# Optimization experiments

Measured on AMD Instinct MI355X. Metric: run time of the kernel, lower is better.

The kernel has to match this reference:

```python
import jax, jax.numpy as jnp
import numpy as np

N_NODES = 100000
N_EDGES = 1600000
D_IN = 128
D_H = 128
D_OUT = 64


def _glorot(key, shape):
    fan_in, fan_out = shape[0], shape[1]
    lim = np.sqrt(6.0 / (fan_in + fan_out)).astype(np.float32)
    return jax.random.uniform(key, shape, jnp.float32, -lim, lim)


def setup_inputs() -> dict:
    key = jax.random.key(0)
    ks = jax.random.split(key, 12)
    x = jax.random.normal(ks[0], (N_NODES, D_IN), jnp.float32)
    edge_index = jax.random.randint(ks[1], (2, N_EDGES), 0, N_NODES, jnp.int64)
    return {
        'x': x,
        'edge_index': edge_index,
        'Wl0': _glorot(ks[2], (D_IN, D_H)),  'bl0': jnp.zeros((D_H,), jnp.float32), 'Wr0': _glorot(ks[3], (D_IN, D_H)),
        'Wl1': _glorot(ks[4], (D_H, D_H)),   'bl1': jnp.zeros((D_H,), jnp.float32), 'Wr1': _glorot(ks[5], (D_H, D_H)),
        'Wl2': _glorot(ks[6], (D_H, D_H)),   'bl2': jnp.zeros((D_H,), jnp.float32), 'Wr2': _glorot(ks[7], (D_H, D_H)),
        'W':   _glorot(ks[8], (D_H, D_OUT)), 'b':   jnp.zeros((D_OUT,), jnp.float32),
    }


def _sage_conv(x, src, dst, inv_deg, Wl, bl, Wr):
    # mean aggregation of neighbor features at dst, then lin_l(agg) + lin_r(x)
    agg = jax.ops.segment_sum(x[src], dst, num_segments=N_NODES)  # [N, d]
    mean = agg * inv_deg  # [N, d]
    return mean @ Wl + bl + x @ Wr


def reference(x, edge_index, Wl0, bl0, Wr0, Wl1, bl1, Wr1, Wl2, bl2, Wr2, W, b):
    src, dst = edge_index[0], edge_index[1]
    deg = jax.ops.segment_sum(jnp.ones((N_EDGES,), jnp.float32), dst, num_segments=N_NODES)
    inv_deg = (1.0 / jnp.maximum(deg, 1.0))[:, None]  # [N, 1]
    h = jax.nn.relu(_sage_conv(x, src, dst, inv_deg, Wl0, bl0, Wr0))
    h = jax.nn.relu(_sage_conv(h, src, dst, inv_deg, Wl1, bl1, Wr1))
    h = jax.nn.relu(_sage_conv(h, src, dst, inv_deg, Wl2, bl2, Wr2))
    return h @ W + b
```

## Files before the change

kernel.cpp:

```cpp
#include <hip/hip_runtime.h>
#include <cstddef>

#define N_NODES 100000
#define N_EDGES 1600000
#define D 128
#define NB 782
#define CAP 3072
#define NBLK 1000
#define CHUNK 1600
#define OROW 784
#define WTOT (6 * 16384 + 8192)

typedef unsigned int u32;
typedef unsigned long long u64;
typedef float f32x4 __attribute__((ext_vector_type(4)));
typedef _Float16 f16x8 __attribute__((ext_vector_type(8)));

__device__ inline f16x8 mk16(u64 a, u64 b) {
  union { u64 q[2]; f16x8 v; } u;
  u.q[0] = a; u.q[1] = b;
  return u.v;
}

__device__ inline void acc8(float* a, uint2 d, float c) {
  a[0] += (float)(d.x & 0xFFu) * c;
  a[1] += (float)((d.x >> 8) & 0xFFu) * c;
  a[2] += (float)((d.x >> 16) & 0xFFu) * c;
  a[3] += (float)(d.x >> 24) * c;
  a[4] += (float)(d.y & 0xFFu) * c;
  a[5] += (float)((d.y >> 8) & 0xFFu) * c;
  a[6] += (float)((d.y >> 16) & 0xFFu) * c;
  a[7] += (float)(d.y >> 24) * c;
}


__global__ __launch_bounds__(256) void k_prep(
    const float* __restrict__ x, unsigned short* __restrict__ x16,
    unsigned char* __restrict__ x8, float* __restrict__ sx,
    const float* __restrict__ w0, const float* __restrict__ w1, const float* __restrict__ w2,
    const float* __restrict__ w3, const float* __restrict__ w4, const float* __restrict__ w5,
    const float* __restrict__ w6, unsigned short* __restrict__ wt16) {
  int bid = blockIdx.x;
  int tid = threadIdx.x;
  if (bid < 6250) {
    int row = bid * 16 + (tid >> 4);
    int sub = tid & 15;
    const float* xr = x + (size_t)row * D + sub * 8;
    float4 v0 = *(const float4*)xr;
    float4 v1 = *(const float4*)(xr + 4);
    float vs[8] = {v0.x, v0.y, v0.z, v0.w, v1.x, v1.y, v1.z, v1.w};
    f16x8 h;
#pragma unroll
    for (int j = 0; j < 8; j++) h[j] = (_Float16)vs[j];
    *(uint4*)(x16 + (size_t)row * D + sub * 8) = __builtin_bit_cast(uint4, h);
    float m = 0.f;
#pragma unroll
    for (int j = 0; j < 8; j++) m = fmaxf(m, fabsf(vs[j]));
#pragma unroll
    for (int off = 1; off < 16; off <<= 1) m = fmaxf(m, __shfl_xor(m, off));
    m = fmaxf(m, 1e-8f);
    float inv = 127.0f / m;
    u64 pk = 0;
#pragma unroll
    for (int j = 0; j < 8; j++) {
      int qi = (int)rintf(vs[j] * inv) + 128;
      pk |= (u64)(u32)(qi & 255) << (8 * j);
    }
    *(u64*)(x8 + (size_t)row * D + sub * 8) = pk;
    if (sub == 0) sx[row] = m / 127.0f;
    return;
  }
  int i = (bid - 6250) * 256 + tid;
  if (i >= WTOT) return;
  float v;
  if (i < 6 * 16384) {
    int m = i >> 14;
    int j = i & 16383;
    int c = j >> 7, k = j & 127;
    const float* w = (m == 0) ? w0 : (m == 1) ? w1 : (m == 2) ? w2
                   : (m == 3) ? w3 : (m == 4) ? w4 : w5;
    v = w[k * 128 + c];
  } else {
    int j = i - 6 * 16384;
    int c = j >> 7, k = j & 127;
    v = w6[k * 64 + c];
  }
  _Float16 h = (_Float16)v;
  wt16[i] = __builtin_bit_cast(unsigned short, h);
}


__global__ __launch_bounds__(256) void k_scatter(const int* __restrict__ src,
                                                 const int* __restrict__ dst,
                                                 u32* __restrict__ binned,
                                                 u32* __restrict__ offs) {
  __shared__ int cnt[NB];
  __shared__ int lbase[NB + 1];
  __shared__ int wsum[256];
  __shared__ u32 stage[CHUNK];
  const int tid = threadIdx.x;
  for (int i = tid; i < NB; i += 256) cnt[i] = 0;
  __syncthreads();
  const int e0 = blockIdx.x * CHUNK;
  for (int e = e0 + tid; e < e0 + CHUNK; e += 256)
    atomicAdd(&cnt[dst[e] >> 7], 1);
  __syncthreads();
  int c[4], s = 0;
#pragma unroll
  for (int j = 0; j < 4; j++) {
    int i = tid * 4 + j;
    c[j] = (i < NB) ? cnt[i] : 0;
    s += c[j];
  }
  wsum[tid] = s;
  __syncthreads();
  for (int off = 1; off < 256; off <<= 1) {
    int t = (tid >= off) ? wsum[tid - off] : 0;
    __syncthreads();
    wsum[tid] += t;
    __syncthreads();
  }
  int run = wsum[tid] - s;
#pragma unroll
  for (int j = 0; j < 4; j++) {
    int i = tid * 4 + j;
    if (i < NB) { lbase[i] = run; run += c[j]; }
  }
  if (tid == 0) lbase[NB] = CHUNK;
  __syncthreads();
  for (int i = tid; i < NB; i += 256) cnt[i] = 0;
  __syncthreads();
  for (int e = e0 + tid; e < e0 + CHUNK; e += 256) {
    int d = dst[e];
    int bkt = d >> 7;
    int l = atomicAdd(&cnt[bkt], 1);
    stage[lbase[bkt] + l] = ((u32)(d & 127) << 17) | (u32)src[e];
  }
  u32* orow = offs + (size_t)blockIdx.x * OROW;
  for (int i = tid; i <= NB; i += 256) orow[i] = (u32)lbase[i];
  __syncthreads();
  u32* bseg = binned + (size_t)blockIdx.x * CHUNK;
  for (int i = tid; i < CHUNK / 4; i += 256)
    *(uint4*)(bseg + i * 4) = *(const uint4*)(stage + i * 4);
}


__global__ __launch_bounds__(256) void k_build(const u32* __restrict__ binned,
                                               const u32* __restrict__ offs,
                                               int* __restrict__ row_start,
                                               int* __restrict__ row_end,
                                               float* __restrict__ inv_deg,
                                               int* __restrict__ csr_src) {
  __shared__ u32 stage[CAP];
  __shared__ int deg[128], sc[128], cur[128];
  __shared__ int fill;
  const int b = blockIdx.x;
  const int tid = threadIdx.x;
  if (tid == 0) fill = 0;
  if (tid < 128) deg[tid] = 0;
  __syncthreads();
  for (int k = tid; k < NBLK; k += 256) {
    const u32* orow = offs + (size_t)k * OROW;
    int o0 = (int)orow[b], o1 = (int)orow[b + 1];
    int n = o1 - o0;
    if (n > 0) {
      int p = atomicAdd(&fill, n);
      const u32* q = binned + (size_t)k * CHUNK + o0;
      for (int j = 0; j < n; ++j) stage[p + j] = q[j];
    }
  }
  __syncthreads();
  const int total = fill;
  for (int e = tid; e < total; e += 256)
    atomicAdd(&deg[stage[e] >> 17], 1);
  __syncthreads();
  int dv = (tid < 128) ? deg[tid] : 0;
  if (tid < 128) sc[tid] = dv;
  __syncthreads();
  for (int off = 1; off < 128; off <<= 1) {
    int t = (tid >= off && tid < 128) ? sc[tid - off] : 0;
    __syncthreads();
    if (tid < 128) sc[tid] += t;
    __syncthreads();
  }
  const int cbase = b * CAP;
  if (tid < 128) {
    int excl = sc[tid] - dv;
    cur[tid] = excl;
    int node = (b << 7) + tid;
    if (node < N_NODES) {
      row_start[node] = cbase + excl;
      row_end[node] = cbase + excl + dv;
      inv_deg[node] = 1.0f / fmaxf((float)dv, 1.0f);
    }
  }
  __syncthreads();
  for (int e = tid; e < total; e += 256) {
    u32 w = stage[e];
    int dl = w >> 17;
    int pos = cbase + atomicAdd(&cur[dl], 1);
    csr_src[pos] = (int)(w & 0x1FFFFu);
  }
}


template <bool BIASED>
__global__ __launch_bounds__(256) void k_agg(const unsigned char* __restrict__ q8,
                                             const float* __restrict__ qs,
                                             const int* __restrict__ row_start,
                                             const int* __restrict__ row_end,
                                             const float* __restrict__ inv_deg,
                                             const int* __restrict__ csr_src,
                                             unsigned short* __restrict__ out16) {
  int node = blockIdx.x * 16 + (threadIdx.x >> 4);
  if (node >= N_NODES) return;
  int sub = threadIdx.x & 15;
  int p0 = row_start[node], p1 = row_end[node];
  float a[8];
#pragma unroll
  for (int j = 0; j < 8; j++) a[j] = 0.f;
  float ssum = 0.f;
  int p = p0;
  for (; p + 8 <= p1; p += 8) {
    int s0 = csr_src[p], s1 = csr_src[p + 1], s2 = csr_src[p + 2], s3 = csr_src[p + 3];
    int s4 = csr_src[p + 4], s5 = csr_src[p + 5], s6 = csr_src[p + 6], s7 = csr_src[p + 7];
    uint2 d0 = *(const uint2*)(q8 + (size_t)s0 * D + sub * 8);
    uint2 d1 = *(const uint2*)(q8 + (size_t)s1 * D + sub * 8);
    uint2 d2 = *(const uint2*)(q8 + (size_t)s2 * D + sub * 8);
    uint2 d3 = *(const uint2*)(q8 + (size_t)s3 * D + sub * 8);
    uint2 d4 = *(const uint2*)(q8 + (size_t)s4 * D + sub * 8);
    uint2 d5 = *(const uint2*)(q8 + (size_t)s5 * D + sub * 8);
    uint2 d6 = *(const uint2*)(q8 + (size_t)s6 * D + sub * 8);
    uint2 d7 = *(const uint2*)(q8 + (size_t)s7 * D + sub * 8);
    float c0 = qs[s0], c1 = qs[s1], c2 = qs[s2], c3 = qs[s3];
    float c4 = qs[s4], c5 = qs[s5], c6 = qs[s6], c7 = qs[s7];
    acc8(a, d0, c0); acc8(a, d1, c1); acc8(a, d2, c2); acc8(a, d3, c3);
    acc8(a, d4, c4); acc8(a, d5, c5); acc8(a, d6, c6); acc8(a, d7, c7);
    if (BIASED) ssum += ((c0 + c1) + (c2 + c3)) + ((c4 + c5) + (c6 + c7));
  }
  for (; p + 2 <= p1; p += 2) {
    int s0 = csr_src[p], s1 = csr_src[p + 1];
    uint2 d0 = *(const uint2*)(q8 + (size_t)s0 * D + sub * 8);
    uint2 d1 = *(const uint2*)(q8 + (size_t)s1 * D + sub * 8);
    float c0 = qs[s0], c1 = qs[s1];
    acc8(a, d0, c0); acc8(a, d1, c1);
    if (BIASED) ssum += c0 + c1;
  }
  if (p < p1) {
    int s0 = csr_src[p];
    uint2 d0 = *(const uint2*)(q8 + (size_t)s0 * D + sub * 8);
    float c0 = qs[s0];
    acc8(a, d0, c0);
    if (BIASED) ssum += c0;
  }
  float scl = inv_deg[node];
  f16x8 o;
#pragma unroll
  for (int j = 0; j < 8; j++) {
    float v = a[j];
    if (BIASED) v -= 128.0f * ssum;
    o[j] = (_Float16)(v * scl);
  }
  *(uint4*)(out16 + (size_t)node * D + sub * 8) = __builtin_bit_cast(uint4, o);
}


__global__ __launch_bounds__(256) void k_gemm(
    const unsigned short* __restrict__ in0, const unsigned short* __restrict__ in1,
    const unsigned short* __restrict__ wt, const float* __restrict__ bias,
    unsigned short* __restrict__ outp,
    unsigned char* __restrict__ h8out, float* __restrict__ shout) {
  __shared__ u64 sI[128][9];
  __shared__ u64 sW[128][9];
  __shared__ u32 rmaxb[128];
  __shared__ unsigned char h8t[128 * 144];

  const int tid = threadIdx.x;
  const int row0 = blockIdx.x * 128;
  const int lane = tid & 63;
  const int w = tid >> 6;
  const int wr = w >> 1, wc = w & 1;
  const int lrow = lane & 15, kb = lane >> 4;
  const int sr = tid >> 2, sq = tid & 3;

  f32x4 acc[4][4];
#pragma unroll
  for (int i = 0; i < 4; i++)
#pragma unroll
    for (int j = 0; j < 4; j++) acc[i][j] = (f32x4){0.f, 0.f, 0.f, 0.f};

  u64 rA[2][2], rW[2][2];

  auto loadA = [&](int ch) {
    const unsigned short* inP = (ch >= 4) ? in1 : in0;
    const int kc = (ch & 3) * 32;
#pragma unroll
    for (int it = 0; it < 2; ++it) {
      int g = row0 + sr + it * 64;
      u64 a = 0, b = 0;
      if (g < N_NODES) {
        const u64* pp = (const u64*)(inP + (size_t)g * D + kc + sq * 8);
        a = pp[0]; b = pp[1];
      }
      rA[it][0] = a; rA[it][1] = b;
    }
  };
  auto loadW = [&](int ch) {
    const int s = ch >> 2;
    const int kc = (ch & 3) * 32;
    const unsigned short* wP = wt + (size_t)s * 16384;
#pragma unroll
    for (int it = 0; it < 2; ++it) {
      int c = sr + it * 64;
      const u64* pp = (const u64*)(wP + (size_t)c * D + kc + sq * 8);
      rW[it][0] = pp[0]; rW[it][1] = pp[1];
    }
  };

  loadA(0); loadW(0);
#pragma unroll
  for (int ch = 0; ch < 8; ++ch) {
    __syncthreads();
#pragma unroll
    for (int it = 0; it < 2; ++it) {
      int r = sr + it * 64;
      sI[r][sq * 2] = rA[it][0]; sI[r][sq * 2 + 1] = rA[it][1];
      sW[r][sq * 2] = rW[it][0]; sW[r][sq * 2 + 1] = rW[it][1];
    }
    __syncthreads();
    if (ch < 7) { loadA(ch + 1); loadW(ch + 1); }

    f16x8 fA[4], fB[4];
#pragma unroll
    for (int rt = 0; rt < 4; ++rt) {
      int rr = wr * 64 + rt * 16 + lrow;
      fA[rt] = mk16(sI[rr][kb * 2], sI[rr][kb * 2 + 1]);
    }
#pragma unroll
    for (int ct = 0; ct < 4; ++ct) {
      int cc = wc * 64 + ct * 16 + lrow;
      fB[ct] = mk16(sW[cc][kb * 2], sW[cc][kb * 2 + 1]);
    }
#pragma unroll
    for (int ct = 0; ct < 4; ++ct)
#pragma unroll
      for (int rt = 0; rt < 4; ++rt)
        acc[rt][ct] = __builtin_amdgcn_mfma_f32_16x16x32_f16(fA[rt], fB[ct], acc[rt][ct], 0, 0, 0);
  }

  if (tid < 128) rmaxb[tid] = 0;
  float bv[4];
#pragma unroll
  for (int ct = 0; ct < 4; ++ct) bv[ct] = bias[wc * 64 + ct * 16 + lrow];
#pragma unroll
  for (int ct = 0; ct < 4; ++ct)
#pragma unroll
    for (int rt = 0; rt < 4; ++rt)
#pragma unroll
      for (int r = 0; r < 4; ++r)
        acc[rt][ct][r] = fmaxf(acc[rt][ct][r] + bv[ct], 0.f);

#pragma unroll
  for (int ct = 0; ct < 4; ++ct) {
    int col = wc * 64 + ct * 16 + lrow;
#pragma unroll
    for (int rt = 0; rt < 4; ++rt) {
#pragma unroll
      for (int r = 0; r < 4; ++r) {
        int g = row0 + wr * 64 + rt * 16 + kb * 4 + r;
        if (g < N_NODES) {
          _Float16 hv = (_Float16)acc[rt][ct][r];
          outp[(size_t)g * D + col] = __builtin_bit_cast(unsigned short, hv);
        }
      }
    }
  }
  __syncthreads();
#pragma unroll
  for (int rt = 0; rt < 4; ++rt) {
#pragma unroll
    for (int r = 0; r < 4; ++r) {
      float m = fmaxf(fmaxf(acc[rt][0][r], acc[rt][1][r]),
                      fmaxf(acc[rt][2][r], acc[rt][3][r]));
      m = fmaxf(m, __shfl_xor(m, 1));
      m = fmaxf(m, __shfl_xor(m, 2));
      m = fmaxf(m, __shfl_xor(m, 4));
      m = fmaxf(m, __shfl_xor(m, 8));
      if (lrow == 0)
        atomicMax(&rmaxb[wr * 64 + rt * 16 + kb * 4 + r], __float_as_uint(m));
    }
  }
  __syncthreads();
#pragma unroll
  for (int rt = 0; rt < 4; ++rt) {
#pragma unroll
    for (int r = 0; r < 4; ++r) {
      int row = wr * 64 + rt * 16 + kb * 4 + r;
      float rm = fmaxf(__uint_as_float(rmaxb[row]), 1e-8f);
      float inv = 255.0f / rm;
#pragma unroll
      for (int ct = 0; ct < 4; ++ct) {
        u32 q = (u32)(acc[rt][ct][r] * inv + 0.5f);
        h8t[row * 144 + wc * 64 + ct * 16 + lrow] = (unsigned char)q;
      }
    }
  }
  __syncthreads();
  for (int idx = tid; idx < 128 * 8; idx += 256) {
    int row = idx >> 3, qq = idx & 7;
    int g = row0 + row;
    if (g < N_NODES)
      *(uint4*)(h8out + (size_t)g * D + qq * 16) =
          *(const uint4*)(h8t + row * 144 + qq * 16);
  }
  if (tid < 128 && row0 + tid < N_NODES)
    shout[row0 + tid] = fmaxf(__uint_as_float(rmaxb[tid]), 1e-8f) / 255.0f;
}


__global__ __launch_bounds__(256) void k_gemm2(
    const unsigned short* __restrict__ in0, const unsigned short* __restrict__ in1,
    const unsigned short* __restrict__ wt, const float* __restrict__ bias,
    const unsigned short* __restrict__ w2, const float* __restrict__ b2,
    float* __restrict__ outp) {
  __shared__ __align__(16) char smem[128 * 33 * 8 + 2 * 128 * 9 * 8];
  u64 (*sH3)[33] = (u64(*)[33])smem;
  u64 (*sI)[9] = (u64(*)[9])(smem + 128 * 33 * 8);
  u64 (*sW)[9] = (u64(*)[9])(smem + 128 * 33 * 8 + 128 * 9 * 8);
  u64 (*sW2)[33] = (u64(*)[33])(smem + 128 * 33 * 8);

  const int tid = threadIdx.x;
  const int row0 = blockIdx.x * 128;
  const int lane = tid & 63;
  const int w = tid >> 6;
  const int wr = w >> 1, wc = w & 1;
  const int lrow = lane & 15, kb = lane >> 4;
  const int sr = tid >> 2, sq = tid & 3;

  f32x4 acc[4][4];
#pragma unroll
  for (int i = 0; i < 4; i++)
#pragma unroll
    for (int j = 0; j < 4; j++) acc[i][j] = (f32x4){0.f, 0.f, 0.f, 0.f};

  u64 rA[2][2], rW[2][2];

  auto loadA = [&](int ch) {
    const unsigned short* inP = (ch >= 4) ? in1 : in0;
    const int kc = (ch & 3) * 32;
#pragma unroll
    for (int it = 0; it < 2; ++it) {
      int g = row0 + sr + it * 64;
      u64 a = 0, b = 0;
      if (g < N_NODES) {
        const u64* pp = (const u64*)(inP + (size_t)g * D + kc + sq * 8);
        a = pp[0]; b = pp[1];
      }
      rA[it][0] = a; rA[it][1] = b;
    }
  };
  auto loadW = [&](int ch) {
    const int s = ch >> 2;
    const int kc = (ch & 3) * 32;
    const unsigned short* wP = wt + (size_t)s * 16384;
#pragma unroll
    for (int it = 0; it < 2; ++it) {
      int c = sr + it * 64;
      const u64* pp = (const u64*)(wP + (size_t)c * D + kc + sq * 8);
      rW[it][0] = pp[0]; rW[it][1] = pp[1];
    }
  };

  loadA(0); loadW(0);
#pragma unroll
  for (int ch = 0; ch < 8; ++ch) {
    __syncthreads();
#pragma unroll
    for (int it = 0; it < 2; ++it) {
      int r = sr + it * 64;
      sI[r][sq * 2] = rA[it][0]; sI[r][sq * 2 + 1] = rA[it][1];
      sW[r][sq * 2] = rW[it][0]; sW[r][sq * 2 + 1] = rW[it][1];
    }
    __syncthreads();
    if (ch < 7) { loadA(ch + 1); loadW(ch + 1); }

    f16x8 fA[4], fB[4];
#pragma unroll
    for (int rt = 0; rt < 4; ++rt) {
      int rr = wr * 64 + rt * 16 + lrow;
      fA[rt] = mk16(sI[rr][kb * 2], sI[rr][kb * 2 + 1]);
    }
#pragma unroll
    for (int ct = 0; ct < 4; ++ct) {
      int cc = wc * 64 + ct * 16 + lrow;
      fB[ct] = mk16(sW[cc][kb * 2], sW[cc][kb * 2 + 1]);
    }
#pragma unroll
    for (int ct = 0; ct < 4; ++ct)
#pragma unroll
      for (int rt = 0; rt < 4; ++rt)
        acc[rt][ct] = __builtin_amdgcn_mfma_f32_16x16x32_f16(fA[rt], fB[ct], acc[rt][ct], 0, 0, 0);
  }

#pragma unroll
  for (int ct = 0; ct < 4; ++ct) {
    int col = wc * 64 + ct * 16 + lrow;
    float bv = bias[col];
#pragma unroll
    for (int rt = 0; rt < 4; ++rt) {
      int rbase = wr * 64 + rt * 16 + kb * 4;
#pragma unroll
      for (int r = 0; r < 4; ++r) {
        float v = fmaxf(acc[rt][ct][r] + bv, 0.f);
        _Float16 hv = (_Float16)v;
        ((unsigned short*)(&sH3[rbase + r][0]))[col] = __builtin_bit_cast(unsigned short, hv);
      }
    }
  }
  __syncthreads();
  for (int idx = tid; idx < 64 * 32; idx += 256) {
    int c = idx >> 5, j = idx & 31;
    sW2[c][j] = ((const u64*)(w2 + (size_t)c * D))[j];
  }
  __syncthreads();

  f32x4 acc2[4][2];
#pragma unroll
  for (int i = 0; i < 4; i++)
#pragma unroll
    for (int j = 0; j < 2; j++) acc2[i][j] = (f32x4){0.f, 0.f, 0.f, 0.f};

#pragma unroll
  for (int kc2 = 0; kc2 < 4; ++kc2) {
    f16x8 fA[4], fB[2];
#pragma unroll
    for (int rt = 0; rt < 4; ++rt) {
      int rr = wr * 64 + rt * 16 + lrow;
      fA[rt] = mk16(sH3[rr][kc2 * 8 + kb * 2], sH3[rr][kc2 * 8 + kb * 2 + 1]);
    }
#pragma unroll
    for (int ct = 0; ct < 2; ++ct) {
      int cc = wc * 32 + ct * 16 + lrow;
      fB[ct] = mk16(sW2[cc][kc2 * 8 + kb * 2], sW2[cc][kc2 * 8 + kb * 2 + 1]);
    }
#pragma unroll
    for (int ct = 0; ct < 2; ++ct)
#pragma unroll
      for (int rt = 0; rt < 4; ++rt)
        acc2[rt][ct] =
            __builtin_amdgcn_mfma_f32_16x16x32_f16(fA[rt], fB[ct], acc2[rt][ct], 0, 0, 0);
  }

#pragma unroll
  for (int ct = 0; ct < 2; ++ct) {
    int col = wc * 32 + ct * 16 + lrow;
    float bv = b2[col];
#pragma unroll
    for (int rt = 0; rt < 4; ++rt) {
#pragma unroll
      for (int r = 0; r < 4; ++r) {
        int g = row0 + wr * 64 + rt * 16 + kb * 4 + r;
        if (g < N_NODES) outp[(size_t)g * 64 + col] = acc2[rt][ct][r] + bv;
      }
    }
  }
}


extern "C" void kernel_launch(void* const* d_in, const int* in_sizes, int n_in,
                              void* d_out, int out_size, void* d_ws, size_t ws_size,
                              hipStream_t stream) {
  const float* x = (const float*)d_in[0];
  const int* edge = (const int*)d_in[1];
  const int* src = edge;
  const int* dst = edge + N_EDGES;
  const float* Wl0 = (const float*)d_in[2];
  const float* bl0 = (const float*)d_in[3];
  const float* Wr0 = (const float*)d_in[4];
  const float* Wl1 = (const float*)d_in[5];
  const float* bl1 = (const float*)d_in[6];
  const float* Wr1 = (const float*)d_in[7];
  const float* Wl2 = (const float*)d_in[8];
  const float* bl2 = (const float*)d_in[9];
  const float* Wr2 = (const float*)d_in[10];
  const float* W = (const float*)d_in[11];
  const float* b = (const float*)d_in[12];
  float* out = (float*)d_out;
  (void)ws_size; (void)n_in; (void)in_sizes; (void)out_size;

  char* ws = (char*)d_ws;
  float* sx = (float*)(ws + (32ll << 10));
  float* sh = (float*)(ws + (448ll << 10));
  int* row_start = (int*)(ws + (1ll << 20));
  int* row_end = (int*)(ws + (2ll << 20));
  float* inv_deg = (float*)(ws + (3ll << 20));
  int* csr_src = (int*)(ws + (4ll << 20));
  u32* offs = (u32*)(ws + (14ll << 20));
  unsigned short* wt16 = (unsigned short*)(ws + (18ll << 20));
  unsigned short* x16 = (unsigned short*)(ws + (19ll << 20));
  unsigned short* agg16 = (unsigned short*)(ws + (45ll << 20));
  unsigned short* hA = (unsigned short*)(ws + (71ll << 20));
  unsigned char* x8 = (unsigned char*)(ws + (97ll << 20));
  unsigned char* h8 = x8;
  u32* binned = (u32*)(ws + (110ll << 20));

  k_prep<<<6250 + (WTOT + 255) / 256, 256, 0, stream>>>(
      x, x16, x8, sx, Wl0, Wr0, Wl1, Wr1, Wl2, Wr2, W, wt16);
  k_scatter<<<NBLK, 256, 0, stream>>>(src, dst, binned, offs);
  k_build<<<NB, 256, 0, stream>>>(binned, offs, row_start, row_end, inv_deg, csr_src);

  const int agg_grid = (N_NODES + 15) / 16;
  const int gemm_grid = (N_NODES + 127) / 128;

  k_agg<true><<<agg_grid, 256, 0, stream>>>(x8, sx, row_start, row_end, inv_deg, csr_src, agg16);
  k_gemm<<<gemm_grid, 256, 0, stream>>>(agg16, x16, wt16 + 0, bl0, hA, h8, sh);
  k_agg<false><<<agg_grid, 256, 0, stream>>>(h8, sh, row_start, row_end, inv_deg, csr_src, agg16);
  k_gemm<<<gemm_grid, 256, 0, stream>>>(agg16, hA, wt16 + 32768, bl1, hA, h8, sh);
  k_agg<false><<<agg_grid, 256, 0, stream>>>(h8, sh, row_start, row_end, inv_deg, csr_src, agg16);
  k_gemm2<<<gemm_grid, 256, 0, stream>>>(agg16, hA, wt16 + 65536, bl2,
                                         wt16 + 98304, b, out);
}
```

Before: 265.4 us.

## Quantize aggregation outputs and self features to int8, dequantize inside GEMM

The aggregation kernel now writes per-row int8-quantized means with a scale instead of fp16, and the GEMMs read int8 for both the aggregated input and the self-feature input, dequantizing to fp16 while staging into shared memory. The fp16 copies of x and of the hidden state are dropped, along with the GEMM's separate fp16 hidden-state store. This cuts global memory traffic on the bandwidth-bound GEMM inputs and writes. In exchange it adds dequantization arithmetic in the GEMM and loses accuracy, because the self term now carries 8-bit precision.

```diff
diff --git a/kernel.cpp b/kernel.cpp
--- a/kernel.cpp
+++ b/kernel.cpp
@@ -33,9 +33,19 @@
   a[7] += (float)(d.y >> 24) * c;
 }
 
+__device__ inline u64 dq4(u32 w, float c, float n) {
+  float f0 = fmaf((float)(w & 0xFFu), c, n);
+  float f1 = fmaf((float)((w >> 8) & 0xFFu), c, n);
+  float f2 = fmaf((float)((w >> 16) & 0xFFu), c, n);
+  float f3 = fmaf((float)(w >> 24), c, n);
+  auto lo = __builtin_amdgcn_cvt_pkrtz(f0, f1);
+  auto hi = __builtin_amdgcn_cvt_pkrtz(f2, f3);
+  return (u64)__builtin_bit_cast(u32, lo) | ((u64)__builtin_bit_cast(u32, hi) << 32);
+}
+
 
 __global__ __launch_bounds__(256) void k_prep(
-    const float* __restrict__ x, unsigned short* __restrict__ x16,
+    const float* __restrict__ x,
     unsigned char* __restrict__ x8, float* __restrict__ sx,
     const float* __restrict__ w0, const float* __restrict__ w1, const float* __restrict__ w2,
     const float* __restrict__ w3, const float* __restrict__ w4, const float* __restrict__ w5,
@@ -49,10 +59,6 @@
     float4 v0 = *(const float4*)xr;
     float4 v1 = *(const float4*)(xr + 4);
     float vs[8] = {v0.x, v0.y, v0.z, v0.w, v1.x, v1.y, v1.z, v1.w};
-    f16x8 h;
-#pragma unroll
-    for (int j = 0; j < 8; j++) h[j] = (_Float16)vs[j];
-    *(uint4*)(x16 + (size_t)row * D + sub * 8) = __builtin_bit_cast(uint4, h);
     float m = 0.f;
 #pragma unroll
     for (int j = 0; j < 8; j++) m = fmaxf(m, fabsf(vs[j]));
@@ -204,14 +210,15 @@
 }
 
 
-template <bool BIASED>
+template <bool BIN, bool BOUT>
 __global__ __launch_bounds__(256) void k_agg(const unsigned char* __restrict__ q8,
                                              const float* __restrict__ qs,
                                              const int* __restrict__ row_start,
                                              const int* __restrict__ row_end,
                                              const float* __restrict__ inv_deg,
                                              const int* __restrict__ csr_src,
-                                             unsigned short* __restrict__ out16) {
+                                             unsigned char* __restrict__ out8,
+                                             float* __restrict__ sout) {
   int node = blockIdx.x * 16 + (threadIdx.x >> 4);
   if (node >= N_NODES) return;
   int sub = threadIdx.x & 15;
@@ -236,7 +243,7 @@
     float c4 = qs[s4], c5 = qs[s5], c6 = qs[s6], c7 = qs[s7];
     acc8(a, d0, c0); acc8(a, d1, c1); acc8(a, d2, c2); acc8(a, d3, c3);
     acc8(a, d4, c4); acc8(a, d5, c5); acc8(a, d6, c6); acc8(a, d7, c7);
-    if (BIASED) ssum += ((c0 + c1) + (c2 + c3)) + ((c4 + c5) + (c6 + c7));
+    if (BIN) ssum += ((c0 + c1) + (c2 + c3)) + ((c4 + c5) + (c6 + c7));
   }
   for (; p + 2 <= p1; p += 2) {
     int s0 = csr_src[p], s1 = csr_src[p + 1];
@@ -244,31 +251,55 @@
     uint2 d1 = *(const uint2*)(q8 + (size_t)s1 * D + sub * 8);
     float c0 = qs[s0], c1 = qs[s1];
     acc8(a, d0, c0); acc8(a, d1, c1);
-    if (BIASED) ssum += c0 + c1;
+    if (BIN) ssum += c0 + c1;
   }
   if (p < p1) {
     int s0 = csr_src[p];
     uint2 d0 = *(const uint2*)(q8 + (size_t)s0 * D + sub * 8);
     float c0 = qs[s0];
     acc8(a, d0, c0);
-    if (BIASED) ssum += c0;
+    if (BIN) ssum += c0;
   }
   float scl = inv_deg[node];
-  f16x8 o;
+  float v[8];
 #pragma unroll
   for (int j = 0; j < 8; j++) {
-    float v = a[j];
-    if (BIASED) v -= 128.0f * ssum;
-    o[j] = (_Float16)(v * scl);
-  }
-  *(uint4*)(out16 + (size_t)node * D + sub * 8) = __builtin_bit_cast(uint4, o);
-}
-
-
+    float t = a[j];
+    if (BIN) t -= 128.0f * ssum;
+    v[j] = t * scl;
+  }
+  float m = 0.f;
+#pragma unroll
+  for (int j = 0; j < 8; j++) m = fmaxf(m, BOUT ? fabsf(v[j]) : v[j]);
+#pragma unroll
+  for (int off = 1; off < 16; off <<= 1) m = fmaxf(m, __shfl_xor(m, off));
+  m = fmaxf(m, 1e-8f);
+  u64 pk = 0;
+  if (BOUT) {
+    float inv = 127.0f / m;
+#pragma unroll
+    for (int j = 0; j < 8; j++) {
+      int qi = (int)rintf(v[j] * inv) + 128;
+      pk |= (u64)(u32)(qi & 255) << (8 * j);
+    }
+  } else {
+    float inv = 255.0f / m;
+#pragma unroll
+    for (int j = 0; j < 8; j++) {
+      u32 qi = (u32)(v[j] * inv + 0.5f);
+      pk |= (u64)(qi & 255) << (8 * j);
+    }
+  }
+  *(u64*)(out8 + (size_t)node * D + sub * 8) = pk;
+  if (sub == 0) sout[node] = m / (BOUT ? 127.0f : 255.0f);
+}
+
+
+template <bool B0, bool B1>
 __global__ __launch_bounds__(256) void k_gemm(
-    const unsigned short* __restrict__ in0, const unsigned short* __restrict__ in1,
+    const unsigned char* __restrict__ in0, const float* __restrict__ s0,
+    const unsigned char* __restrict__ in1, const float* __restrict__ s1,
     const unsigned short* __restrict__ wt, const float* __restrict__ bias,
-    unsigned short* __restrict__ outp,
     unsigned char* __restrict__ h8out, float* __restrict__ shout) {
   __shared__ u64 sI[128][9];
   __shared__ u64 sW[128][9];
@@ -289,20 +320,23 @@
 #pragma unroll
     for (int j = 0; j < 4; j++) acc[i][j] = (f32x4){0.f, 0.f, 0.f, 0.f};
 
-  u64 rA[2][2], rW[2][2];
+  uint2 rd[2]; float rc[2];
+  u64 rW[2][2];
 
   auto loadA = [&](int ch) {
-    const unsigned short* inP = (ch >= 4) ? in1 : in0;
+    const unsigned char* inP = (ch >= 4) ? in1 : in0;
+    const float* sP = (ch >= 4) ? s1 : s0;
     const int kc = (ch & 3) * 32;
 #pragma unroll
     for (int it = 0; it < 2; ++it) {
       int g = row0 + sr + it * 64;
-      u64 a = 0, b = 0;
+      uint2 d = make_uint2(0, 0);
+      float c = 0.f;
       if (g < N_NODES) {
-        const u64* pp = (const u64*)(inP + (size_t)g * D + kc + sq * 8);
-        a = pp[0]; b = pp[1];
+        d = *(const uint2*)(inP + (size_t)g * D + kc + sq * 8);
+        c = sP[g];
       }
-      rA[it][0] = a; rA[it][1] = b;
+      rd[it] = d; rc[it] = c;
     }
   };
   auto loadW = [&](int ch) {
@@ -320,11 +354,15 @@
   loadA(0); loadW(0);
 #pragma unroll
   for (int ch = 0; ch < 8; ++ch) {
+    const bool biased = (ch < 4) ? B0 : B1;
     __syncthreads();
 #pragma unroll
     for (int it = 0; it < 2; ++it) {
       int r = sr + it * 64;
-      sI[r][sq * 2] = rA[it][0]; sI[r][sq * 2 + 1] = rA[it][1];
+      float c = rc[it];
+      float n = biased ? -128.0f * c : 0.0f;
+      sI[r][sq * 2] = dq4(rd[it].x, c, n);
+      sI[r][sq * 2 + 1] = dq4(rd[it].y, c, n);
       sW[r][sq * 2] = rW[it][0]; sW[r][sq * 2 + 1] = rW[it][1];
     }
     __syncthreads();
@@ -359,22 +397,6 @@
 #pragma unroll
       for (int r = 0; r < 4; ++r)
         acc[rt][ct][r] = fmaxf(acc[rt][ct][r] + bv[ct], 0.f);
-
-#pragma unroll
-  for (int ct = 0; ct < 4; ++ct) {
-    int col = wc * 64 + ct * 16 + lrow;
-#pragma unroll
-    for (int rt = 0; rt < 4; ++rt) {
-#pragma unroll
-      for (int r = 0; r < 4; ++r) {
-        int g = row0 + wr * 64 + rt * 16 + kb * 4 + r;
-        if (g < N_NODES) {
-          _Float16 hv = (_Float16)acc[rt][ct][r];
-          outp[(size_t)g * D + col] = __builtin_bit_cast(unsigned short, hv);
-        }
-      }
-    }
-  }
   __syncthreads();
 #pragma unroll
   for (int rt = 0; rt < 4; ++rt) {
@@ -418,8 +440,10 @@
 }
 
 
+template <bool B0, bool B1>
 __global__ __launch_bounds__(256) void k_gemm2(
-    const unsigned short* __restrict__ in0, const unsigned short* __restrict__ in1,
+    const unsigned char* __restrict__ in0, const float* __restrict__ s0,
+    const unsigned char* __restrict__ in1, const float* __restrict__ s1,
     const unsigned short* __restrict__ wt, const float* __restrict__ bias,
     const unsigned short* __restrict__ w2, const float* __restrict__ b2,
     float* __restrict__ outp) {
@@ -443,20 +467,23 @@
 #pragma unroll
     for (int j = 0; j < 4; j++) acc[i][j] = (f32x4){0.f, 0.f, 0.f, 0.f};
 
-  u64 rA[2][2], rW[2][2];
+  uint2 rd[2]; float rc[2];
+  u64 rW[2][2];
 
   auto loadA = [&](int ch) {
-    const unsigned short* inP = (ch >= 4) ? in1 : in0;
+    const unsigned char* inP = (ch >= 4) ? in1 : in0;
+    const float* sP = (ch >= 4) ? s1 : s0;
     const int kc = (ch & 3) * 32;
 #pragma unroll
     for (int it = 0; it < 2; ++it) {
       int g = row0 + sr + it * 64;
-      u64 a = 0, b = 0;
+      uint2 d = make_uint2(0, 0);
+      float c = 0.f;
       if (g < N_NODES) {
-        const u64* pp = (const u64*)(inP + (size_t)g * D + kc + sq * 8);
-        a = pp[0]; b = pp[1];
+        d = *(const uint2*)(inP + (size_t)g * D + kc + sq * 8);
+        c = sP[g];
       }
-      rA[it][0] = a; rA[it][1] = b;
+      rd[it] = d; rc[it] = c;
     }
   };
   auto loadW = [&](int ch) {
@@ -474,11 +501,15 @@
   loadA(0); loadW(0);
 #pragma unroll
   for (int ch = 0; ch < 8; ++ch) {
+    const bool biased = (ch < 4) ? B0 : B1;
     __syncthreads();
 #pragma unroll
     for (int it = 0; it < 2; ++it) {
       int r = sr + it * 64;
-      sI[r][sq * 2] = rA[it][0]; sI[r][sq * 2 + 1] = rA[it][1];
+      float c = rc[it];
+      float n = biased ? -128.0f * c : 0.0f;
+      sI[r][sq * 2] = dq4(rd[it].x, c, n);
+      sI[r][sq * 2 + 1] = dq4(rd[it].y, c, n);
       sW[r][sq * 2] = rW[it][0]; sW[r][sq * 2 + 1] = rW[it][1];
     }
     __syncthreads();
@@ -589,34 +620,38 @@
   (void)ws_size; (void)n_in; (void)in_sizes; (void)out_size;
 
   char* ws = (char*)d_ws;
-  float* sx = (float*)(ws + (32ll << 10));
-  float* sh = (float*)(ws + (448ll << 10));
-  int* row_start = (int*)(ws + (1ll << 20));
-  int* row_end = (int*)(ws + (2ll << 20));
-  float* inv_deg = (float*)(ws + (3ll << 20));
-  int* csr_src = (int*)(ws + (4ll << 20));
-  u32* offs = (u32*)(ws + (14ll << 20));
-  unsigned short* wt16 = (unsigned short*)(ws + (18ll << 20));
-  unsigned short* x16 = (unsigned short*)(ws + (19ll << 20));
-  unsigned short* agg16 = (unsigned short*)(ws + (45ll << 20));
-  unsigned short* hA = (unsigned short*)(ws + (71ll << 20));
-  unsigned char* x8 = (unsigned char*)(ws + (97ll << 20));
-  unsigned char* h8 = x8;
-  u32* binned = (u32*)(ws + (110ll << 20));
+  float* sx = (float*)(ws);
+  float* sh = (float*)(ws + (512ll << 10));
+  float* sa = (float*)(ws + (1ll << 20));
+  int* row_start = (int*)(ws + (2ll << 20));
+  int* row_end = (int*)(ws + (3ll << 20));
+  float* inv_deg = (float*)(ws + (4ll << 20));
+  int* csr_src = (int*)(ws + (5ll << 20));
+  u32* offs = (u32*)(ws + (15ll << 20));
+  unsigned short* wt16 = (unsigned short*)(ws + (19ll << 20));
+  unsigned char* agg8 = (unsigned char*)(ws + (20ll << 20));
+  unsigned char* x8 = (unsigned char*)(ws + (33ll << 20));
+  unsigned char* h8 = (unsigned char*)(ws + (46ll << 20));
+  u32* binned = (u32*)(ws + (59ll << 20));
 
   k_prep<<<6250 + (WTOT + 255) / 256, 256, 0, stream>>>(
-      x, x16, x8, sx, Wl0, Wr0, Wl1, Wr1, Wl2, Wr2, W, wt16);
+      x, x8, sx, Wl0, Wr0, Wl1, Wr1, Wl2, Wr2, W, wt16);
   k_scatter<<<NBLK, 256, 0, stream>>>(src, dst, binned, offs);
   k_build<<<NB, 256, 0, stream>>>(binned, offs, row_start, row_end, inv_deg, csr_src);
 
   const int agg_grid = (N_NODES + 15) / 16;
   const int gemm_grid = (N_NODES + 127) / 128;
 
-  k_agg<true><<<agg_grid, 256, 0, stream>>>(x8, sx, row_start, row_end, inv_deg, csr_src, agg16);
-  k_gemm<<<gemm_grid, 256, 0, stream>>>(agg16, x16, wt16 + 0, bl0, hA, h8, sh);
-  k_agg<false><<<agg_grid, 256, 0, stream>>>(h8, sh, row_start, row_end, inv_deg, csr_src, agg16);
-  k_gemm<<<gemm_grid, 256, 0, stream>>>(agg16, hA, wt16 + 32768, bl1, hA, h8, sh);
-  k_agg<false><<<agg_grid, 256, 0, stream>>>(h8, sh, row_start, row_end, inv_deg, csr_src, agg16);
-  k_gemm2<<<gemm_grid, 256, 0, stream>>>(agg16, hA, wt16 + 65536, bl2,
-                                         wt16 + 98304, b, out);
-}
+  k_agg<true, true><<<agg_grid, 256, 0, stream>>>(
+      x8, sx, row_start, row_end, inv_deg, csr_src, agg8, sa);
+  k_gemm<true, true><<<gemm_grid, 256, 0, stream>>>(
+      agg8, sa, x8, sx, wt16 + 0, bl0, h8, sh);
+  k_agg<false, false><<<agg_grid, 256, 0, stream>>>(
+      h8, sh, row_start, row_end, inv_deg, csr_src, agg8, sa);
+  k_gemm<false, false><<<gemm_grid, 256, 0, stream>>>(
+      agg8, sa, h8, sh, wt16 + 32768, bl1, h8, sh);
+  k_agg<false, false><<<agg_grid, 256, 0, stream>>>(
+      h8, sh, row_start, row_end, inv_deg, csr_src, agg8, sa);
+  k_gemm2<false, false><<<gemm_grid, 256, 0, stream>>>(
+      agg8, sa, h8, sh, wt16 + 65536, bl2, wt16 + 98304, b, out);
+}
```

Result: faster. 250.6 us (-5.6%).
